# Kernel tuning notes

Hardware: AMD Instinct MI355X
Metric: run time of the kernel (lower is better)

The kernel has to match this reference:

```python
import jax, jax.numpy as jnp
import numpy as np

B, L, E, H = 4, 4096, 1024, 16
D = E // H
SQRT_D = float(np.sqrt(D))


def _g(x):
    # torch: softplus(x, beta=5) ** 2
    sp = jax.nn.softplus(5.0 * x) / 5.0
    return sp * sp


def setup_inputs() -> dict:
    key = jax.random.key(0)
    ks = jax.random.split(key, 7)
    s = 1.0 / np.sqrt(E)
    x = jax.random.normal(ks[0], (B, L, E), jnp.float32)
    Wq = jax.random.normal(ks[1], (E, E), jnp.float32) * s
    bq = jax.random.normal(ks[2], (E,), jnp.float32) * s
    Wk = jax.random.normal(ks[3], (E, E), jnp.float32) * s
    bk = jax.random.normal(ks[4], (E,), jnp.float32) * s
    Wv = jax.random.normal(ks[5], (E, E), jnp.float32) * s
    bv = jax.random.normal(ks[6], (E,), jnp.float32) * s
    return {"x": x, "Wq": Wq, "bq": bq, "Wk": Wk, "bk": bk, "Wv": Wv, "bv": bv}


def _fast_linear_attn(q, k, v):
    # q,k,v: [B,S,H,D]
    Ls = q.shape[1]
    # RALA-style global-query rescaling of K
    q_global = q.mean(axis=1, keepdims=True) / SQRT_D          # [B,1,H,D]
    logits = jnp.einsum('bihd,blhd->bihl', q_global, k)        # [B,1,H,L]
    alpha = jax.nn.softmax(logits, axis=-1) * Ls               # [B,1,H,L]
    alpha = jnp.transpose(alpha[:, 0], (0, 2, 1))[..., None]   # [B,L,H,1]
    k = k * alpha
    gq, gk = _g(q), _g(k)
    gmq, gmk = _g(-q), _g(-k)
    # symmetric / antisymmetric KV accumulation: state [B,H,D,D]
    gk_v = jnp.einsum('bshd,bshv->bhdv', gk, v)
    gmk_v = jnp.einsum('bshd,bshv->bhdv', gmk, v)
    num = (jnp.einsum('bshd,bhdv->bshv', gq, gk_v)
           + jnp.einsum('bshd,bhdv->bshv', gmq, gmk_v))        # [B,S,H,D]
    den = (jnp.einsum('bshd,bhd->bsh', gq, gk.sum(axis=1))
           + jnp.einsum('bshd,bhd->bsh', gmq, gmk.sum(axis=1)))
    return num / (den[..., None] + 1e-6)


def reference(x, Wq, bq, Wk, bk, Wv, bv):
    q = (x @ Wq + bq).reshape(B, L, H, D)
    k = (x @ Wk + bk).reshape(B, L, H, D)
    v = (x @ Wv + bv).reshape(B, L, H, D)
    out = _fast_linear_attn(q, k, v)  # [B,L,H,D]
    return out.reshape(B, L, E)
```

## Files before the change

kernel.cpp:

```cpp
#include <hip/hip_runtime.h>
#include <hip/hip_bf16.h>
#include <math.h>

#define B_ 4
#define L_ 4096
#define E_ 1024
#define H_ 16
#define D_ 64
#define M_ (B_*L_)

typedef __attribute__((ext_vector_type(8))) short s8;
typedef __attribute__((ext_vector_type(4))) float f4;

__device__ __forceinline__ float gfun(float x) {
  float z = fminf(5.0f * x, 60.0f);
  float sp = 0.2f * __logf(1.0f + __expf(z));
  return sp * sp;
}

__device__ __forceinline__ unsigned short f2bf(float v) {
  __hip_bfloat16 h = __float2bfloat16(v);
  return *reinterpret_cast<unsigned short*>(&h);
}
__device__ __forceinline__ float bf2f(unsigned short u) {
  __hip_bfloat16 h = *reinterpret_cast<__hip_bfloat16*>(&u);
  return __bfloat162float(h);
}

__device__ __forceinline__ void gload16(const void* g, void* l) {
  __builtin_amdgcn_global_load_lds(
      (const __attribute__((address_space(1))) void*)g,
      (__attribute__((address_space(3))) void*)l, 16, 0, 0);
}

__global__ __launch_bounds__(256) void split_x(
    const float* __restrict__ x, unsigned short* __restrict__ Ah,
    float* __restrict__ xsum)
{
  int blk = blockIdx.x, t = threadIdx.x;
  int r0 = blk * 64, b = r0 >> 12;
  int c4 = t * 4;
  float4 cs = {0.f, 0.f, 0.f, 0.f};
  for (int r = 0; r < 64; ++r) {
    int row = r0 + r;
    float4 x4 = *(const float4*)(x + (size_t)row * E_ + c4);
    ushort4 hi, lo;
    unsigned short h;
    h = f2bf(x4.x); hi.x = h; lo.x = f2bf(x4.x - bf2f(h));
    h = f2bf(x4.y); hi.y = h; lo.y = f2bf(x4.y - bf2f(h));
    h = f2bf(x4.z); hi.z = h; lo.z = f2bf(x4.z - bf2f(h));
    h = f2bf(x4.w); hi.w = h; lo.w = f2bf(x4.w - bf2f(h));
    *(ushort4*)&Ah[(size_t)row * 2048 + c4]        = hi;
    *(ushort4*)&Ah[(size_t)row * 2048 + 1024 + c4] = lo;
    cs.x += x4.x; cs.y += x4.y; cs.z += x4.z; cs.w += x4.w;
  }
  atomicAdd(&xsum[b * E_ + c4 + 0], cs.x);
  atomicAdd(&xsum[b * E_ + c4 + 1], cs.y);
  atomicAdd(&xsum[b * E_ + c4 + 2], cs.z);
  atomicAdd(&xsum[b * E_ + c4 + 3], cs.w);
}

__global__ __launch_bounds__(256) void split_wT(
    const float* __restrict__ Wq, const float* __restrict__ Wk,
    const float* __restrict__ Wv, const float* __restrict__ bq,
    const float* __restrict__ xsum,
    unsigned short* __restrict__ Bt, float* __restrict__ qg)
{
  int z = blockIdx.z;
  const float* W = (z == 0) ? Wq : (z == 1) ? Wk : Wv;
  __shared__ float tile[32][33];
  int t = threadIdx.x;
  int tx = t & 31, ty = t >> 5;
  int k0 = blockIdx.x * 32, n0 = blockIdx.y * 32;
  #pragma unroll
  for (int i = 0; i < 4; ++i)
    tile[ty + i*8][tx] = W[(size_t)(k0 + ty + i*8) * 1024 + n0 + tx];
  __syncthreads();
  unsigned short* Bz = Bt + (size_t)z * 2097152;
  #pragma unroll
  for (int i = 0; i < 4; ++i) {
    int n = n0 + ty + i*8, kk = k0 + tx;
    float v = tile[tx][ty + i*8];
    unsigned short h = f2bf(v);
    Bz[(size_t)n * 2048 + kk]        = h;
    Bz[(size_t)n * 2048 + 1024 + kk] = f2bf(v - bf2f(h));
  }
  if (z == 0 && t < 128) {
    int n = t & 31, b = t >> 5;
    float dot = 0.f;
    #pragma unroll
    for (int kk = 0; kk < 32; ++kk)
      dot += xsum[b * E_ + k0 + kk] * tile[kk][n];
    float val = dot * (1.0f / (L_ * 8.0f));
    if (k0 == 0) val += bq[n0 + n] * 0.125f;
    atomicAdd(&qg[b * E_ + n0 + n], val);
  }
}

#define PRIO1() __builtin_amdgcn_s_setprio(1)
#define PRIO0() __builtin_amdgcn_s_setprio(0)
#define BARR() do { asm volatile("" ::: "memory"); \
                    __builtin_amdgcn_s_barrier(); \
                    asm volatile("" ::: "memory"); } while (0)
#define WAITL0() asm volatile("s_waitcnt lgkmcnt(0)" ::: "memory")
#define WAITV(n) asm volatile("s_waitcnt vmcnt(" n ")" ::: "memory")

#define STAGE_A(buf, kofs) do { \
  const unsigned short* g_ = gA + (kofs); \
  char* d_ = dA0 + (buf) * 32768; \
  gload16(g_,          d_); \
  gload16(g_ + 131072, d_ +  8192); \
  gload16(g_ + 262144, d_ + 16384); \
  gload16(g_ + 393216, d_ + 24576); \
} while (0)

#define STAGE_B(buf, kofs) do { \
  const unsigned short* g_ = gB + (kofs); \
  char* d_ = dB0 + (buf) * 32768; \
  gload16(g_,          d_); \
  gload16(g_ + 131072, d_ +  8192); \
  gload16(g_ + 262144, d_ + 16384); \
  gload16(g_ + 393216, d_ + 24576); \
} while (0)

#define LDA(buf, mh) do { \
  const char* p_ = shb + (buf) * 32768 + arow + (mh) * 8192; \
  _Pragma("unroll") \
  for (int ii = 0; ii < 4; ++ii) { \
    aF[ii][0] = *(const s8*)(p_ + ii * 2048 + c0); \
    aF[ii][1] = *(const s8*)(p_ + ii * 2048 + c1); \
  } \
} while (0)

#define LDB(buf, nh) do { \
  const char* p_ = shb + 65536 + (buf) * 32768 + brow + (nh) * 4096; \
  _Pragma("unroll") \
  for (int jj = 0; jj < 2; ++jj) { \
    bF[(nh)*2+jj][0] = *(const s8*)(p_ + jj * 2048 + c0); \
    bF[(nh)*2+jj][1] = *(const s8*)(p_ + jj * 2048 + c1); \
  } \
} while (0)

#define MFMAQ(mh, nh) do { \
  _Pragma("unroll") \
  for (int ii = 0; ii < 4; ++ii) \
    _Pragma("unroll") \
    for (int jj = 0; jj < 2; ++jj) { \
      acc[(mh)*4+ii][(nh)*2+jj] = __builtin_amdgcn_mfma_f32_16x16x32_bf16( \
          aF[ii][0], bF[(nh)*2+jj][0], acc[(mh)*4+ii][(nh)*2+jj], 0, 0, 0); \
      acc[(mh)*4+ii][(nh)*2+jj] = __builtin_amdgcn_mfma_f32_16x16x32_bf16( \
          aF[ii][1], bF[(nh)*2+jj][1], acc[(mh)*4+ii][(nh)*2+jj], 0, 0, 0); \
    } \
} while (0)

#define TILE4(buf, doStage, kB_, kA_, vmN) do { \
   \
  LDA(buf, 0); LDB(buf, 0); LDB(buf, 1); \
  BARR(); WAITL0(); \
  PRIO1(); MFMAQ(0, 0); PRIO0(); \
  BARR(); \
   \
  if (doStage) STAGE_B(buf, kB_); \
  BARR(); \
  PRIO1(); MFMAQ(0, 1); PRIO0(); \
  BARR(); \
   \
  LDA(buf, 1); \
  BARR(); WAITL0(); \
  PRIO1(); MFMAQ(1, 0); PRIO0(); \
  BARR(); \
   \
  if (doStage) STAGE_A(buf, kA_); \
  BARR(); \
  PRIO1(); MFMAQ(1, 1); PRIO0(); \
  WAITV(vmN); \
  BARR(); \
} while (0)

__global__ __launch_bounds__(512, 2) void qkv_mfma(
    const unsigned short* __restrict__ Ah, const unsigned short* __restrict__ Bt,
    const float* __restrict__ bq, const float* __restrict__ bk,
    const float* __restrict__ bv, const float* __restrict__ qg,
    float* __restrict__ aexp, float* __restrict__ denom,
    float* __restrict__ qo, float* __restrict__ ko, float* __restrict__ vo)
{
  __shared__ unsigned short sh[65536];

  const int t  = threadIdx.x;
  const int li = blockIdx.x;
  const int xc = li & 7;
  const int idx = li >> 3;
  const int z   = idx >> 5;
  const int rem = idx & 31;
  const int bm = (xc * 8 + (rem >> 2)) * 256;
  const int bn = (rem & 3) * 256;

  const float* bias = (z == 0) ? bq : (z == 1) ? bk : bv;
  float* out = (z == 0) ? qo : (z == 1) ? ko : vo;
  const unsigned short* Bz = Bt + (size_t)z * 2097152;

  const int srow = t >> 3;
  const int scol = ((t & 7) ^ (srow & 7)) * 8;
  const unsigned short* gA = Ah + (size_t)(bm + srow) * 2048 + scol;
  const unsigned short* gB = Bz + (size_t)(bn + srow) * 2048 + scol;
  char* const shb = (char*)sh;
  char* const dA0 = shb +         t * 16;
  char* const dB0 = shb + 65536 + t * 16;

  const int lane = t & 63, wid = t >> 6;
  const int wm = wid >> 2, wn = wid & 3;
  const int fr = lane & 15, fq = lane >> 4;
  const int c0 = ((fq)     ^ (fr & 7)) * 16;
  const int c1 = ((fq + 4) ^ (fr & 7)) * 16;
  const int arow = (wm * 128 + fr) * 128;
  const int brow = (wn *  64 + fr) * 128;

  f4 acc[8][4] = {};
  s8 aF[4][2], bF[4][2];

  STAGE_B(0, 0);  STAGE_A(0, 0);
  STAGE_B(1, 64); STAGE_A(1, 64);
  WAITV("8");
  BARR();

  #pragma unroll 1
  for (int it = 0; it < 23; ++it) {
    const int t2 = 2 * it + 2, t3 = 2 * it + 3;
    const int kA2 = (t2 < 16) ? t2 * 64 : t2 * 64 - 1024;
    const int kB2 = (t2 < 32) ? t2 * 64 : t2 * 64 - 2048;
    const int kA3 = (t3 < 16) ? t3 * 64 : t3 * 64 - 1024;
    const int kB3 = (t3 < 32) ? t3 * 64 : t3 * 64 - 2048;
    TILE4(0, true, kB2, kA2, "8");
    TILE4(1, true, kB3, kA3, "8");
  }
  TILE4(0, false, 0, 0, "0");
  TILE4(1, false, 0, 0, "0");

  float bv4[4];
  #pragma unroll
  for (int j = 0; j < 4; ++j) bv4[j] = bias[bn + wn * 64 + j * 16 + fr];
  #pragma unroll
  for (int i = 0; i < 8; ++i) {
    const int mrow = bm + wm * 128 + i * 16 + fq * 4;
    #pragma unroll
    for (int j = 0; j < 4; ++j) {
      const int ncol = bn + wn * 64 + j * 16 + fr;
      #pragma unroll
      for (int r = 0; r < 4; ++r)
        out[(size_t)(mrow + r) * E_ + ncol] = acc[i][j][r] + bv4[j];
    }
  }

  if (z == 1) {
    const int b_ = bm >> 12;
    const int h  = (bn >> 6) + wn;
    const int bh = b_ * 16 + h;
    float qgv[4];
    #pragma unroll
    for (int j = 0; j < 4; ++j) qgv[j] = qg[bh * 64 + j * 16 + fr];
    float partial[8][4];
    #pragma unroll
    for (int i = 0; i < 8; ++i)
      #pragma unroll
      for (int r = 0; r < 4; ++r) {
        float p = 0.f;
        #pragma unroll
        for (int j = 0; j < 4; ++j)
          p += qgv[j] * (acc[i][j][r] + bv4[j]);
        p += __shfl_xor(p, 1);
        p += __shfl_xor(p, 2);
        p += __shfl_xor(p, 4);
        p += __shfl_xor(p, 8);
        partial[i][r] = p;
      }
    if (fr == 0) {
      const int lbase = (bm & 4095) + wm * 128 + fq * 4;
      float s = 0.f;
      #pragma unroll
      for (int i = 0; i < 8; ++i)
        #pragma unroll
        for (int r = 0; r < 4; ++r) {
          float e = __expf(partial[i][r]);
          aexp[(size_t)bh * 4096 + lbase + i * 16 + r] = e;
          s += e;
        }
      atomicAdd(&denom[bh], s);
    }
  }
}

__global__ __launch_bounds__(256) void state_part(
    const float* __restrict__ k, const float* __restrict__ v,
    const float* __restrict__ aexp, const float* __restrict__ denom,
    float* __restrict__ Spart, float* __restrict__ SMpart,
    float* __restrict__ kpart, float* __restrict__ kmpart)
{
  int bh = blockIdx.x; int b = bh >> 4, h = bh & 15;
  int c = blockIdx.y;
  int l0 = c * 256;
  float scale = (float)L_ / denom[bh];
  __shared__ float gk[2][16][64], gmk[2][16][64], vt[2][16][64];
  int t = threadIdx.x;
  int lr = t >> 4, cc = (t & 15) * 4;
  int vg = (t & 7) * 8, dg = ((t >> 3) & 15) * 4, team = t >> 7;
  float acc[4][8] = {}, accm[4][8] = {};
  float sgk[4] = {}, sgmk[4] = {};

  for (int lt = 0; lt < 256; lt += 16) {
    int cur = (lt >> 4) & 1;
    int l = l0 + lt + lr;
    size_t off = (size_t)(b*L_ + l) * E_ + h*64 + cc;
    float4 k4 = *(const float4*)(k + off);
    float4 v4 = *(const float4*)(v + off);
    float av = aexp[(size_t)bh * L_ + l] * scale;
    float4 g4, m4;
    g4.x = gfun( k4.x*av); m4.x = gfun(-k4.x*av);
    g4.y = gfun( k4.y*av); m4.y = gfun(-k4.y*av);
    g4.z = gfun( k4.z*av); m4.z = gfun(-k4.z*av);
    g4.w = gfun( k4.w*av); m4.w = gfun(-k4.w*av);
    *(float4*)&gk [cur][lr][cc] = g4;
    *(float4*)&gmk[cur][lr][cc] = m4;
    *(float4*)&vt [cur][lr][cc] = v4;
    __syncthreads();
    #pragma unroll
    for (int l2 = 0; l2 < 8; ++l2) {
      int ls = team * 8 + l2;
      float4 ga = *(float4*)&gk [cur][ls][dg];
      float4 ma = *(float4*)&gmk[cur][ls][dg];
      float4 vA = *(float4*)&vt [cur][ls][vg];
      float4 vB = *(float4*)&vt [cur][ls][vg + 4];
      float gv[4] = {ga.x, ga.y, ga.z, ga.w};
      float mv[4] = {ma.x, ma.y, ma.z, ma.w};
      float vv[8] = {vA.x, vA.y, vA.z, vA.w, vB.x, vB.y, vB.z, vB.w};
      if ((t & 7) == 0) {
        #pragma unroll
        for (int i = 0; i < 4; ++i) { sgk[i] += gv[i]; sgmk[i] += mv[i]; }
      }
      #pragma unroll
      for (int i = 0; i < 4; ++i)
        #pragma unroll
        for (int j = 0; j < 8; ++j) {
          acc [i][j] += gv[i] * vv[j];
          accm[i][j] += mv[i] * vv[j];
        }
    }
  }

  int p = c * 2 + team;
  size_t pb = ((size_t)(p*64 + bh)) * 4096 + (size_t)dg * 64 + vg;
  #pragma unroll
  for (int i = 0; i < 4; ++i) {
    *(float4*)&Spart [pb + i*64]     = *(float4*)&acc [i][0];
    *(float4*)&Spart [pb + i*64 + 4] = *(float4*)&acc [i][4];
    *(float4*)&SMpart[pb + i*64]     = *(float4*)&accm[i][0];
    *(float4*)&SMpart[pb + i*64 + 4] = *(float4*)&accm[i][4];
  }
  if ((t & 7) == 0) {
    #pragma unroll
    for (int i = 0; i < 4; ++i) {
      kpart [(p*64 + bh)*64 + dg + i] = sgk[i];
      kmpart[(p*64 + bh)*64 + dg + i] = sgmk[i];
    }
  }
}

__global__ __launch_bounds__(256) void state_reduce(
    const float* __restrict__ Spart, const float* __restrict__ SMpart,
    const float* __restrict__ kpart, const float* __restrict__ kmpart,
    float* __restrict__ S, float* __restrict__ Sm,
    float* __restrict__ ksum, float* __restrict__ kmsum)
{
  int bh = blockIdx.x, seg = blockIdx.y, t = threadIdx.x;
  int idx = seg * 1024 + t * 4;
  float4 s = {0,0,0,0}, sm = {0,0,0,0};
  #pragma unroll
  for (int p = 0; p < 32; ++p) {
    float4 a = *(const float4*)&Spart [((size_t)(p*64 + bh))*4096 + idx];
    float4 c = *(const float4*)&SMpart[((size_t)(p*64 + bh))*4096 + idx];
    s.x += a.x; s.y += a.y; s.z += a.z; s.w += a.w;
    sm.x += c.x; sm.y += c.y; sm.z += c.z; sm.w += c.w;
  }
  *(float4*)&S [(size_t)bh*4096 + idx] = s;
  *(float4*)&Sm[(size_t)bh*4096 + idx] = sm;
  if (seg == 0 && t < 64) {
    float a = 0.f, c = 0.f;
    #pragma unroll
    for (int p = 0; p < 32; ++p) {
      a += kpart [(p*64 + bh)*64 + t];
      c += kmpart[(p*64 + bh)*64 + t];
    }
    ksum [bh*64 + t] = a;
    kmsum[bh*64 + t] = c;
  }
}

__global__ __launch_bounds__(128, 4) void out_kernel(
    const float* __restrict__ q,
    const float* __restrict__ S, const float* __restrict__ Sm,
    const float* __restrict__ ksum, const float* __restrict__ kmsum,
    float* __restrict__ out)
{
  int bh = blockIdx.x; int b = bh >> 4, h = bh & 15;
  int l0 = blockIdx.y * 64;
  __shared__ float Gq[64][64], Gm[64][64];
  int t = threadIdx.x;

  int lr = t >> 1, dq = (t & 1) * 32;
  const float4* qp = (const float4*)(q + (size_t)(b*L_ + l0 + lr)*E_ + h*64 + dq);
  #pragma unroll
  for (int j = 0; j < 8; ++j) {
    float4 qv = qp[j];
    float vals[4] = {qv.x, qv.y, qv.z, qv.w};
    #pragma unroll
    for (int jj = 0; jj < 4; ++jj) {
      int dd = dq + j*4 + jj;
      Gq[dd][lr] = gfun(vals[jj]);
      Gm[dd][lr] = gfun(-vals[jj]);
    }
  }
  __syncthreads();

  int tn = (t & 7) * 8, tm = (t >> 3) * 4;
  const float* Sp   = S  + (size_t)bh*4096;
  const float* Smp  = Sm + (size_t)bh*4096;
  const float* ksp  = ksum  + bh*64;
  const float* kmsp = kmsum + bh*64;
  float acc[4][8] = {};
  float den[4] = {};
  #pragma unroll 2
  for (int kk = 0; kk < 64; ++kk) {
    float4 ga = *(const float4*)&Gq[kk][tm];
    float4 ma = *(const float4*)&Gm[kk][tm];
    float4 s0 = *(const float4*)&Sp [kk*64 + tn];
    float4 s1 = *(const float4*)&Sp [kk*64 + tn + 4];
    float4 m0 = *(const float4*)&Smp[kk*64 + tn];
    float4 m1 = *(const float4*)&Smp[kk*64 + tn + 4];
    float ksv = ksp[kk], kmv = kmsp[kk];
    float gv[4] = {ga.x, ga.y, ga.z, ga.w};
    float mv[4] = {ma.x, ma.y, ma.z, ma.w};
    float sv[8] = {s0.x, s0.y, s0.z, s0.w, s1.x, s1.y, s1.z, s1.w};
    float smv[8] = {m0.x, m0.y, m0.z, m0.w, m1.x, m1.y, m1.z, m1.w};
    #pragma unroll
    for (int i = 0; i < 4; ++i) {
      #pragma unroll
      for (int j = 0; j < 8; ++j)
        acc[i][j] += gv[i]*sv[j] + mv[i]*smv[j];
      den[i] += gv[i]*ksv + mv[i]*kmv;
    }
  }

  #pragma unroll
  for (int i = 0; i < 4; ++i) {
    float r = 1.0f / (den[i] + 1e-6f);
    float4 o0, o1;
    o0.x = acc[i][0]*r; o0.y = acc[i][1]*r; o0.z = acc[i][2]*r; o0.w = acc[i][3]*r;
    o1.x = acc[i][4]*r; o1.y = acc[i][5]*r; o1.z = acc[i][6]*r; o1.w = acc[i][7]*r;
    size_t ro = (size_t)(b*L_ + l0 + tm + i)*E_ + h*64 + tn;
    *(float4*)(out + ro)     = o0;
    *(float4*)(out + ro + 4) = o1;
  }
}

extern "C" void kernel_launch(void* const* d_in, const int* in_sizes, int n_in,
                              void* d_out, int out_size, void* d_ws, size_t ws_size,
                              hipStream_t stream) {
  const float* x  = (const float*)d_in[0];
  const float* Wq = (const float*)d_in[1];
  const float* bq = (const float*)d_in[2];
  const float* Wk = (const float*)d_in[3];
  const float* bk = (const float*)d_in[4];
  const float* Wv = (const float*)d_in[5];
  const float* bv = (const float*)d_in[6];
  float* out = (float*)d_out;
  float* ws  = (float*)d_ws;

  float* q      = ws;
  float* k      = ws + 16777216;
  float* qg     = ws + 33554432;
  float* denom  = ws + 33558528;
  float* xsum   = ws + 33558592;
  float* S      = ws + 33562688;
  float* Sm     = ws + 33824832;
  float* ksum   = ws + 34086976;
  float* kmsum  = ws + 34091072;
  float* aexp   = ws + 34095168;
  unsigned short* Ah = (unsigned short*)(ws + 34357312);
  unsigned short* Bt = (unsigned short*)(ws + 51134528);
  float* Spart  = ws + 34357312;
  float* SMpart = ws + 42745920;
  float* kpart  = ws + 51134528;
  float* kmpart = ws + 51265600;
  float* v      = out;

  hipMemsetAsync(qg, 0, 8256 * sizeof(float), stream);

  split_x<<<256, 256, 0, stream>>>(x, Ah, xsum);
  split_wT<<<dim3(32, 32, 3), 256, 0, stream>>>(Wq, Wk, Wv, bq, xsum, Bt, qg);
  qkv_mfma<<<dim3(768), 512, 0, stream>>>(Ah, Bt, bq, bk, bv, qg,
                                          aexp, denom, q, k, v);
  state_part<<<dim3(B_*H_, 16), 256, 0, stream>>>(k, v, aexp, denom,
                                                  Spart, SMpart, kpart, kmpart);
  state_reduce<<<dim3(B_*H_, 4), 256, 0, stream>>>(Spart, SMpart, kpart, kmpart,
                                                   S, Sm, ksum, kmsum);
  out_kernel<<<dim3(B_*H_, 64), 128, 0, stream>>>(q, S, Sm, ksum, kmsum, out);
}
```

Before: 672.2 us.

## Compute KV state partials with split-bf16 MFMA instead of scalar FMAs

The state_part kernel now computes g(k)·v and g(-k)·v outer-product sums with bf16 MFMA instructions. Each fp32 operand is split into hi/lo bf16 halves stacked along the K dimension (hi·hi + hi·lo + lo·hi), kept in an XOR-swizzled LDS layout. Chunks shrink to 128 rows and the grid doubles to 32 chunks, so state_reduce still sees 32 partials. The aim is to replace the FP32 scalar FMA inner loop with matrix-core throughput. It risks small precision loss because the lo·lo term is dropped, and the ksum partials are now summed from bf16 hi/lo values.

```diff
diff --git a/kernel.cpp b/kernel.cpp
--- a/kernel.cpp
+++ b/kernel.cpp
@@ -295,72 +295,124 @@
     float* __restrict__ Spart, float* __restrict__ SMpart,
     float* __restrict__ kpart, float* __restrict__ kmpart)
 {
-  int bh = blockIdx.x; int b = bh >> 4, h = bh & 15;
-  int c = blockIdx.y;
-  int l0 = c * 256;
-  float scale = (float)L_ / denom[bh];
-  __shared__ float gk[2][16][64], gmk[2][16][64], vt[2][16][64];
-  int t = threadIdx.x;
-  int lr = t >> 4, cc = (t & 15) * 4;
-  int vg = (t & 7) * 8, dg = ((t >> 3) & 15) * 4, team = t >> 7;
-  float acc[4][8] = {}, accm[4][8] = {};
-  float sgk[4] = {}, sgmk[4] = {};
-
-  for (int lt = 0; lt < 256; lt += 16) {
-    int cur = (lt >> 4) & 1;
-    int l = l0 + lt + lr;
-    size_t off = (size_t)(b*L_ + l) * E_ + h*64 + cc;
-    float4 k4 = *(const float4*)(k + off);
-    float4 v4 = *(const float4*)(v + off);
-    float av = aexp[(size_t)bh * L_ + l] * scale;
-    float4 g4, m4;
-    g4.x = gfun( k4.x*av); m4.x = gfun(-k4.x*av);
-    g4.y = gfun( k4.y*av); m4.y = gfun(-k4.y*av);
-    g4.z = gfun( k4.z*av); m4.z = gfun(-k4.z*av);
-    g4.w = gfun( k4.w*av); m4.w = gfun(-k4.w*av);
-    *(float4*)&gk [cur][lr][cc] = g4;
-    *(float4*)&gmk[cur][lr][cc] = m4;
-    *(float4*)&vt [cur][lr][cc] = v4;
-    __syncthreads();
-    #pragma unroll
-    for (int l2 = 0; l2 < 8; ++l2) {
-      int ls = team * 8 + l2;
-      float4 ga = *(float4*)&gk [cur][ls][dg];
-      float4 ma = *(float4*)&gmk[cur][ls][dg];
-      float4 vA = *(float4*)&vt [cur][ls][vg];
-      float4 vB = *(float4*)&vt [cur][ls][vg + 4];
-      float gv[4] = {ga.x, ga.y, ga.z, ga.w};
-      float mv[4] = {ma.x, ma.y, ma.z, ma.w};
-      float vv[8] = {vA.x, vA.y, vA.z, vA.w, vB.x, vB.y, vB.z, vB.w};
-      if ((t & 7) == 0) {
+  __shared__ unsigned short lds[49152];
+  const int bh = blockIdx.x, b = bh >> 4, h = bh & 15;
+  const int c = blockIdx.y;
+  const int l0 = c * 128;
+  const float scale = (float)L_ / denom[bh];
+  const int t = threadIdx.x;
+
+  {
+    const int lp = t >> 2, c4 = t & 3;
+    const size_t r0 = (size_t)(b * L_ + l0 + 2 * lp) * E_ + h * 64;
+    float4 k0[4], k1[4], v0[4], v1[4];
+    #pragma unroll
+    for (int i = 0; i < 4; ++i) {
+      const int col = c4 * 4 + i * 16;
+      k0[i] = *(const float4*)(k + r0 + col);
+      k1[i] = *(const float4*)(k + r0 + E_ + col);
+      v0[i] = *(const float4*)(v + r0 + col);
+      v1[i] = *(const float4*)(v + r0 + E_ + col);
+    }
+    const float av0 = aexp[(size_t)bh * L_ + l0 + 2 * lp]     * scale;
+    const float av1 = aexp[(size_t)bh * L_ + l0 + 2 * lp + 1] * scale;
+    const int usl = 2 * lp;
+    #pragma unroll
+    for (int i = 0; i < 4; ++i) {
+      const float ke[4] = {k0[i].x, k0[i].y, k0[i].z, k0[i].w};
+      const float ko[4] = {k1[i].x, k1[i].y, k1[i].z, k1[i].w};
+      const float ve[4] = {v0[i].x, v0[i].y, v0[i].z, v0[i].w};
+      const float vo[4] = {v1[i].x, v1[i].y, v1[i].z, v1[i].w};
+      #pragma unroll
+      for (int j = 0; j < 4; ++j) {
+        const int d  = c4 * 4 + i * 16 + j;
+        const int rb = d * 256, x7 = d & 7;
+        const int ph = rb + (((usl      ) >> 3) ^ x7) * 8 + (usl & 7);
+        const int pl = rb + (((usl + 128) >> 3) ^ x7) * 8 + (usl & 7);
+        const float ge = gfun( ke[j] * av0), go = gfun( ko[j] * av1);
+        const float me = gfun(-ke[j] * av0), mo = gfun(-ko[j] * av1);
+        unsigned short eh, oh;
+        unsigned int w;
+        eh = f2bf(ge); oh = f2bf(go);
+        w = (unsigned)eh | ((unsigned)oh << 16);
+        *(unsigned int*)&lds[ph] = w;
+        eh = f2bf(ge - bf2f(eh)); oh = f2bf(go - bf2f(oh));
+        w = (unsigned)eh | ((unsigned)oh << 16);
+        *(unsigned int*)&lds[pl] = w;
+        eh = f2bf(me); oh = f2bf(mo);
+        w = (unsigned)eh | ((unsigned)oh << 16);
+        *(unsigned int*)&lds[16384 + ph] = w;
+        eh = f2bf(me - bf2f(eh)); oh = f2bf(mo - bf2f(oh));
+        w = (unsigned)eh | ((unsigned)oh << 16);
+        *(unsigned int*)&lds[16384 + pl] = w;
+        eh = f2bf(ve[j]); oh = f2bf(vo[j]);
+        w = (unsigned)eh | ((unsigned)oh << 16);
+        *(unsigned int*)&lds[32768 + ph] = w;
+        eh = f2bf(ve[j] - bf2f(eh)); oh = f2bf(vo[j] - bf2f(oh));
+        w = (unsigned)eh | ((unsigned)oh << 16);
+        *(unsigned int*)&lds[32768 + pl] = w;
+      }
+    }
+  }
+  __syncthreads();
+
+  {
+    const int wid = t >> 6, lane = t & 63;
+    const int s = wid >> 1, dh = wid & 1;
+    const int fr = lane & 15, fq = lane >> 4;
+    const unsigned short* AT = lds + s * 16384;
+    const unsigned short* VT = lds + 32768;
+    f4 acc[2][4] = {};
+    #pragma unroll
+    for (int ks = 0; ks < 12; ++ks) {
+      const int seg = ks >> 2, loc = ks & 3;
+      const int ac = loc * 32 + fq * 8 + ((seg == 2) ? 128 : 0);
+      const int bc = loc * 32 + fq * 8 + ((seg == 1) ? 128 : 0);
+      s8 aF[2], bF[4];
+      #pragma unroll
+      for (int m = 0; m < 2; ++m) {
+        const int row = dh * 32 + m * 16 + fr;
+        aF[m] = *(const s8*)&AT[row * 256 + ((ac >> 3) ^ (row & 7)) * 8 + (ac & 7)];
+      }
+      #pragma unroll
+      for (int n = 0; n < 4; ++n) {
+        const int row = n * 16 + fr;
+        bF[n] = *(const s8*)&VT[row * 256 + ((bc >> 3) ^ (row & 7)) * 8 + (bc & 7)];
+      }
+      #pragma unroll
+      for (int m = 0; m < 2; ++m)
         #pragma unroll
-        for (int i = 0; i < 4; ++i) { sgk[i] += gv[i]; sgmk[i] += mv[i]; }
-      }
-      #pragma unroll
-      for (int i = 0; i < 4; ++i)
+        for (int n = 0; n < 4; ++n)
+          acc[m][n] = __builtin_amdgcn_mfma_f32_16x16x32_bf16(
+              aF[m], bF[n], acc[m][n], 0, 0, 0);
+    }
+    float* Sp = (s == 0) ? Spart : SMpart;
+    const size_t pb = ((size_t)(c * 64 + bh)) * 4096;
+    #pragma unroll
+    for (int m = 0; m < 2; ++m)
+      #pragma unroll
+      for (int n = 0; n < 4; ++n)
         #pragma unroll
-        for (int j = 0; j < 8; ++j) {
-          acc [i][j] += gv[i] * vv[j];
-          accm[i][j] += mv[i] * vv[j];
+        for (int r = 0; r < 4; ++r) {
+          const int d  = dh * 32 + m * 16 + fq * 4 + r;
+          const int vv = n * 16 + fr;
+          Sp[pb + d * 64 + vv] = acc[m][n][r];
         }
-    }
-  }
-
-  int p = c * 2 + team;
-  size_t pb = ((size_t)(p*64 + bh)) * 4096 + (size_t)dg * 64 + vg;
-  #pragma unroll
-  for (int i = 0; i < 4; ++i) {
-    *(float4*)&Spart [pb + i*64]     = *(float4*)&acc [i][0];
-    *(float4*)&Spart [pb + i*64 + 4] = *(float4*)&acc [i][4];
-    *(float4*)&SMpart[pb + i*64]     = *(float4*)&accm[i][0];
-    *(float4*)&SMpart[pb + i*64 + 4] = *(float4*)&accm[i][4];
-  }
-  if ((t & 7) == 0) {
-    #pragma unroll
-    for (int i = 0; i < 4; ++i) {
-      kpart [(p*64 + bh)*64 + dg + i] = sgk[i];
-      kmpart[(p*64 + bh)*64 + dg + i] = sgmk[i];
-    }
+  }
+
+  if (t < 128) {
+    const int isM = t >> 6, d = t & 63;
+    const unsigned short* R = lds + isM * 16384 + d * 256;
+    const int x7 = d & 7;
+    float sum = 0.f;
+    #pragma unroll
+    for (int sl = 0; sl < 32; ++sl) {
+      s8 w8 = *(const s8*)&R[(sl ^ x7) * 8];
+      #pragma unroll
+      for (int e = 0; e < 8; ++e)
+        sum += bf2f((unsigned short)w8[e]);
+    }
+    (isM ? kmpart : kpart)[(c * 64 + bh) * 64 + d] = sum;
   }
 }
 
@@ -498,7 +550,7 @@
   split_wT<<<dim3(32, 32, 3), 256, 0, stream>>>(Wq, Wk, Wv, bq, xsum, Bt, qg);
   qkv_mfma<<<dim3(768), 512, 0, stream>>>(Ah, Bt, bq, bk, bv, qg,
                                           aexp, denom, q, k, v);
-  state_part<<<dim3(B_*H_, 16), 256, 0, stream>>>(k, v, aexp, denom,
+  state_part<<<dim3(B_*H_, 32), 256, 0, stream>>>(k, v, aexp, denom,
                                                   Spart, SMpart, kpart, kmpart);
   state_reduce<<<dim3(B_*H_, 4), 256, 0, stream>>>(Spart, SMpart, kpart, kmpart,
                                                    S, Sm, ksum, kmsum);
```

Result: no change. 676.5 us (+0.6%).
